# Performance work log

Hardware: AMD Instinct MI355X
Metric: run time of the kernel (lower is better)

Reference implementation:

```python
import jax, jax.numpy as jnp
import numpy as np

N_NODES = 100000
N_EDGES = 1600000
D = 64


def setup_inputs() -> dict:
    key = jax.random.key(0)
    k1, k2, k3 = jax.random.split(key, 3)
    x = jax.random.normal(k1, (N_NODES, D), dtype=jnp.float32)
    edge_index = jax.random.randint(k2, (2, N_EDGES), 0, N_NODES, dtype=jnp.int32)
    W = jax.random.normal(k3, (D, D), dtype=jnp.float32) * 0.05  # linear weight [out_dim, in_dim]
    b = jnp.zeros((D,), dtype=jnp.float32)
    return {"x": x, "edge_index": edge_index, "W": W, "b": b}


def reference(x, edge_index, W, b):
    n = x.shape[0]
    # add self loops
    loops = jnp.arange(n, dtype=edge_index.dtype)
    src = jnp.concatenate([edge_index[0], loops])
    dst = jnp.concatenate([edge_index[1], loops])
    # in-degree (counting self loops) via scatter-add of ones onto dst
    deg = jax.ops.segment_sum(jnp.ones_like(src, dtype=x.dtype), dst, num_segments=n)
    deg_inv_sqrt = jnp.where(deg > 0, jax.lax.rsqrt(jnp.maximum(deg, 1.0)) * (deg > 0), 0.0)
    deg_inv_sqrt = jnp.where(deg > 0, deg ** -0.5, 0.0)
    # per-edge symmetric normalization, gather-scale-scatter
    norm = deg_inv_sqrt[src] * deg_inv_sqrt[dst]  # [E+N]
    msgs = x[src] * norm[:, None]                  # [E+N, D] big irregular gather
    out = jax.ops.segment_sum(msgs, dst, num_segments=n)  # scatter-add to nodes
    # dense linear
    return out @ W.T + b
```

## Files before the change

kernel.cpp:

```cpp
#include <hip/hip_runtime.h>


#define BSHIFT 7
#define BNODES 128
#define CAP 3072
#define EPB 4096
#define SMEM_BYTES 32768

__device__ inline unsigned short f2b_rn(float f) {
    unsigned u = __float_as_uint(f);
    unsigned r = u + 0x7FFFu + ((u >> 16) & 1u);
    return (unsigned short)(r >> 16);
}
__device__ inline float b2f(unsigned short h) {
    return __uint_as_float(((unsigned)h) << 16);
}

__global__ __launch_bounds__(256) void fused_gemm_scatter_kernel(
    const float* __restrict__ x, const float* __restrict__ W,
    ushort4* __restrict__ yh,
    const int* __restrict__ ei, int* __restrict__ gcur,
    unsigned int* __restrict__ grec,
    int n, int e, int nbuck, int sblocks) {
    __shared__ __align__(16) unsigned char smem[SMEM_BYTES];
    int t = threadIdx.x;

    if ((int)blockIdx.x < sblocks) {
        unsigned int* lrec = (unsigned int*)smem;
        unsigned short* lbk = (unsigned short*)(smem + 16384);
        int* lh = (int*)(smem + 24576);
        int* lbase = lh + nbuck;
        for (int i = t; i < nbuck; i += 256) lh[i] = 0;
        __syncthreads();
        int e0 = blockIdx.x * EPB;
        int m = e - e0;
        if (m > EPB) m = EPB;
        for (int i = t; i < m; i += 256) {
            int g = e0 + i;
            int s = ei[g];
            int d = ei[e + g];
            int b = d >> BSHIFT;
            lrec[i] = ((unsigned int)s << BSHIFT) | (unsigned int)(d & (BNODES - 1));
            lbk[i] = (unsigned short)b;
            atomicAdd(&lh[b], 1);
        }
        __syncthreads();
        for (int b = t; b < nbuck; b += 256) {
            int c = lh[b];
            lbase[b] = c ? atomicAdd(&gcur[b], c) : 0;
            lh[b] = 0;
        }
        __syncthreads();
        for (int i = t; i < m; i += 256) {
            int b = lbk[i];
            int pos = lbase[b] + atomicAdd(&lh[b], 1);
            if (pos < CAP)
                grec[(size_t)b * CAP + pos] = lrec[i];
        }
    } else {
        float4* At4 = (float4*)smem;
        float4* Wt4 = (float4*)(smem + 16384);
        int m0 = ((int)blockIdx.x - sblocks) * 64;

#pragma unroll
        for (int j = 0; j < 4; ++j) {
            int idx = t + j * 256;
            int k = idx & 63;
            int r = idx >> 6;
            float4 wv;
            wv.x = W[(size_t)(4 * r + 0) * 64 + k];
            wv.y = W[(size_t)(4 * r + 1) * 64 + k];
            wv.z = W[(size_t)(4 * r + 2) * 64 + k];
            wv.w = W[(size_t)(4 * r + 3) * 64 + k];
            Wt4[k * 16 + (r ^ (k & 15))] = wv;
            float4 av;
            int gm = m0 + 4 * r;
            av.x = (gm + 0 < n) ? x[(size_t)(gm + 0) * 64 + k] : 0.f;
            av.y = (gm + 1 < n) ? x[(size_t)(gm + 1) * 64 + k] : 0.f;
            av.z = (gm + 2 < n) ? x[(size_t)(gm + 2) * 64 + k] : 0.f;
            av.w = (gm + 3 < n) ? x[(size_t)(gm + 3) * 64 + k] : 0.f;
            At4[k * 16 + (r ^ (k & 15))] = av;
        }
        __syncthreads();

        int tx = t & 15, ty = t >> 4;
        float acc[4][4];
#pragma unroll
        for (int i = 0; i < 4; ++i)
#pragma unroll
            for (int j = 0; j < 4; ++j) acc[i][j] = 0.f;

#pragma unroll 8
        for (int k = 0; k < 64; ++k) {
            float4 a = At4[k * 16 + (ty ^ (k & 15))];
            float4 w = Wt4[k * 16 + (tx ^ (k & 15))];
            float av[4] = {a.x, a.y, a.z, a.w};
            float wv[4] = {w.x, w.y, w.z, w.w};
#pragma unroll
            for (int i = 0; i < 4; ++i)
#pragma unroll
                for (int j = 0; j < 4; ++j) acc[i][j] += av[i] * wv[j];
        }

#pragma unroll
        for (int i = 0; i < 4; ++i) {
            int gm = m0 + ty * 4 + i;
            if (gm < n) {
                ushort4 h;
                h.x = f2b_rn(acc[i][0]);
                h.y = f2b_rn(acc[i][1]);
                h.z = f2b_rn(acc[i][2]);
                h.w = f2b_rn(acc[i][3]);
                yh[(size_t)gm * 16 + tx] = h;
            }
        }
    }
}

__global__ __launch_bounds__(256) void dnorm_kernel(
    const unsigned int* __restrict__ grec, const int* __restrict__ gcur,
    float* __restrict__ dnorm, int n) {
    __shared__ int lh[BNODES];
    int t = threadIdx.x;
    int b = blockIdx.x;
    size_t base = (size_t)b * CAP;
    int cnt = gcur[b];
    if (cnt > CAP) cnt = CAP;
    if (t < BNODES) lh[t] = 0;
    __syncthreads();
    for (int i = t; i < cnt; i += 256)
        atomicAdd(&lh[grec[base + i] & (BNODES - 1)], 1);
    __syncthreads();
    if (t < BNODES) {
        int node = (b << BSHIFT) + t;
        if (node < n) dnorm[node] = rsqrtf((float)lh[t] + 1.0f);
    }
}

__global__ __launch_bounds__(512, 4) void csr_gather_kernel(
    const unsigned int* __restrict__ grec, const int* __restrict__ gcur,
    const ushort4* __restrict__ yh, const float* __restrict__ dnorm,
    const float* __restrict__ bias,
    float4* __restrict__ out, int n) {
    __shared__ unsigned int sorted[CAP];
    __shared__ int lh[BNODES];
    __shared__ int ls[BNODES + 1];
    __shared__ int wtot;
    int t = threadIdx.x;
    int b = blockIdx.x;
    size_t base = (size_t)b * CAP;
    int cnt = gcur[b];
    if (cnt > CAP) cnt = CAP;
    int node0 = b << BSHIFT;

    if (t < BNODES) lh[t] = 0;
    __syncthreads();
    for (int i = t; i < cnt; i += 512)
        atomicAdd(&lh[grec[base + i] & (BNODES - 1)], 1);
    __syncthreads();
    int c = 0, ex = 0;
    if (t < BNODES) {
        c = lh[t];
        int lane64 = t & 63;
        int v = c;
#pragma unroll
        for (int o = 1; o < 64; o <<= 1) {
            int u = __shfl_up(v, o, 64);
            if (lane64 >= o) v += u;
        }
        if (t == 63) wtot = v;
        ex = v - c;
    }
    __syncthreads();
    if (t >= 64 && t < BNODES) ex += wtot;
    if (t < BNODES) {
        ls[t] = ex;
        lh[t] = 0;
        if (t == BNODES - 1) ls[BNODES] = ex + c;
    }
    __syncthreads();
    for (int i = t; i < cnt; i += 512) {
        unsigned int r = grec[base + i];
        int nd = r & (BNODES - 1);
        int pos = ls[nd] + atomicAdd(&lh[nd], 1);
        sorted[pos] = r >> BSHIFT;
    }
    __syncthreads();

    int wave = t >> 6;
    int lane = t & 63;
    int grp = lane >> 4;
    int fq = lane & 15;
    float4 bb = ((const float4*)bias)[fq];
    for (int i = 0; i < 16; ++i) {
        int nd = wave * 16 + i;
        int node = node0 + nd;
        if (node >= n) break;
        int beg = ls[nd];
        int end = ls[nd + 1];
        float dn = rsqrtf((float)(end - beg) + 1.0f);
        float4 acc = {0.f, 0.f, 0.f, 0.f};
        if (grp == 0) {
            ushort4 h = yh[(size_t)node * 16 + fq];
            acc.x = dn * b2f(h.x); acc.y = dn * b2f(h.y);
            acc.z = dn * b2f(h.z); acc.w = dn * b2f(h.w);
        }
        int j = beg + grp;
        for (; j + 12 < end; j += 16) {
            int s0 = (int)sorted[j];
            int s1 = (int)sorted[j + 4];
            int s2 = (int)sorted[j + 8];
            int s3 = (int)sorted[j + 12];
            ushort4 h0 = yh[(size_t)s0 * 16 + fq];
            ushort4 h1 = yh[(size_t)s1 * 16 + fq];
            ushort4 h2 = yh[(size_t)s2 * 16 + fq];
            ushort4 h3 = yh[(size_t)s3 * 16 + fq];
            float d0 = dnorm[s0];
            float d1 = dnorm[s1];
            float d2 = dnorm[s2];
            float d3 = dnorm[s3];
            acc.x += d0 * b2f(h0.x); acc.x += d1 * b2f(h1.x);
            acc.x += d2 * b2f(h2.x); acc.x += d3 * b2f(h3.x);
            acc.y += d0 * b2f(h0.y); acc.y += d1 * b2f(h1.y);
            acc.y += d2 * b2f(h2.y); acc.y += d3 * b2f(h3.y);
            acc.z += d0 * b2f(h0.z); acc.z += d1 * b2f(h1.z);
            acc.z += d2 * b2f(h2.z); acc.z += d3 * b2f(h3.z);
            acc.w += d0 * b2f(h0.w); acc.w += d1 * b2f(h1.w);
            acc.w += d2 * b2f(h2.w); acc.w += d3 * b2f(h3.w);
        }
        for (; j < end; j += 4) {
            int s = (int)sorted[j];
            ushort4 h = yh[(size_t)s * 16 + fq];
            float d0 = dnorm[s];
            acc.x += d0 * b2f(h.x); acc.y += d0 * b2f(h.y);
            acc.z += d0 * b2f(h.z); acc.w += d0 * b2f(h.w);
        }
        for (int m = 16; m < 64; m <<= 1) {
            acc.x += __shfl_xor(acc.x, m);
            acc.y += __shfl_xor(acc.y, m);
            acc.z += __shfl_xor(acc.z, m);
            acc.w += __shfl_xor(acc.w, m);
        }
        if (lane < 16) {
            float4 o;
            o.x = acc.x * dn + bb.x;
            o.y = acc.y * dn + bb.y;
            o.z = acc.z * dn + bb.z;
            o.w = acc.w * dn + bb.w;
            out[(size_t)node * 16 + lane] = o;
        }
    }
}

extern "C" void kernel_launch(void* const* d_in, const int* in_sizes, int n_in,
                              void* d_out, int out_size, void* d_ws, size_t ws_size,
                              hipStream_t stream) {
    const float* x    = (const float*)d_in[0];
    const int*   ei   = (const int*)d_in[1];
    const float* W    = (const float*)d_in[2];
    const float* bias = (const float*)d_in[3];
    float* out = (float*)d_out;

    int n = in_sizes[0] / 64;
    int e = in_sizes[1] / 2;
    int nbuck = (n + BNODES - 1) / BNODES;

    auto align = [](size_t v) { return (v + 255) & ~(size_t)255; };
    char* p = (char*)d_ws;
    int* gcur = (int*)p;                    p += align((size_t)nbuck * 4);
    unsigned int* grec = (unsigned int*)p;  p += align((size_t)nbuck * CAP * 4);
    float* dnorm = (float*)p;               p += align((size_t)n * 4);
    ushort4* yh = (ushort4*)p;

    int sblocks = (e + EPB - 1) / EPB;
    int gblocks = (n + 63) / 64;

    hipMemsetAsync(gcur, 0, (size_t)nbuck * 4, stream);
    fused_gemm_scatter_kernel<<<sblocks + gblocks, 256, 0, stream>>>(
        x, W, yh, ei, gcur, grec, n, e, nbuck, sblocks);
    dnorm_kernel<<<nbuck, 256, 0, stream>>>(grec, gcur, dnorm, n);
    csr_gather_kernel<<<nbuck, 512, 0, stream>>>(grec, gcur, yh, dnorm, bias,
                                                 (float4*)out, n);
}
```

Baseline: 165.9 us.

## Compute dense x·Wᵀ with split-bf16 MFMA instead of shared-memory FP32 FMA

Replaces the LDS-tiled FP32 FMA GEMM in the transform blocks with 16x16x32 bf16 MFMA instructions. Each operand is split into a hi/lo bf16 pair and three MFMAs are issued so the result stays close to FP32 accuracy. Operands now load straight from global memory into registers, removing the shared-memory staging and the block barrier. This trades scalar FMA work for matrix-core throughput, at the cost of extra split arithmetic and W being reloaded per wave.

```diff
diff --git a/kernel.cpp b/kernel.cpp
--- a/kernel.cpp
+++ b/kernel.cpp
@@ -7,6 +7,9 @@
 #define EPB 4096
 #define SMEM_BYTES 32768
 
+typedef short bf16x8 __attribute__((ext_vector_type(8)));
+typedef float f32x4 __attribute__((ext_vector_type(4)));
+
 __device__ inline unsigned short f2b_rn(float f) {
     unsigned u = __float_as_uint(f);
     unsigned r = u + 0x7FFFu + ((u >> 16) & 1u);
@@ -14,6 +17,24 @@
 }
 __device__ inline float b2f(unsigned short h) {
     return __uint_as_float(((unsigned)h) << 16);
+}
+
+__device__ inline void split8(float4 a, float4 b, bf16x8* hi, bf16x8* lo) {
+    float f[8] = {a.x, a.y, a.z, a.w, b.x, b.y, b.z, b.w};
+    union U { unsigned u[4]; bf16x8 v; } uh, ul;
+#pragma unroll
+    for (int i = 0; i < 4; ++i) {
+        unsigned u0 = __float_as_uint(f[2 * i]);
+        unsigned u1 = __float_as_uint(f[2 * i + 1]);
+        uh.u[i] = (u0 >> 16) | (u1 & 0xFFFF0000u);
+        float r0 = f[2 * i]     - __uint_as_float(u0 & 0xFFFF0000u);
+        float r1 = f[2 * i + 1] - __uint_as_float(u1 & 0xFFFF0000u);
+        unsigned v0 = __float_as_uint(r0);
+        unsigned v1 = __float_as_uint(r1);
+        ul.u[i] = (v0 >> 16) | (v1 & 0xFFFF0000u);
+    }
+    *hi = uh.v;
+    *lo = ul.v;
 }
 
 __global__ __launch_bounds__(256) void fused_gemm_scatter_kernel(
@@ -58,60 +79,46 @@
                 grec[(size_t)b * CAP + pos] = lrec[i];
         }
     } else {
-        float4* At4 = (float4*)smem;
-        float4* Wt4 = (float4*)(smem + 16384);
-        int m0 = ((int)blockIdx.x - sblocks) * 64;
-
-#pragma unroll
-        for (int j = 0; j < 4; ++j) {
-            int idx = t + j * 256;
-            int k = idx & 63;
-            int r = idx >> 6;
-            float4 wv;
-            wv.x = W[(size_t)(4 * r + 0) * 64 + k];
-            wv.y = W[(size_t)(4 * r + 1) * 64 + k];
-            wv.z = W[(size_t)(4 * r + 2) * 64 + k];
-            wv.w = W[(size_t)(4 * r + 3) * 64 + k];
-            Wt4[k * 16 + (r ^ (k & 15))] = wv;
-            float4 av;
-            int gm = m0 + 4 * r;
-            av.x = (gm + 0 < n) ? x[(size_t)(gm + 0) * 64 + k] : 0.f;
-            av.y = (gm + 1 < n) ? x[(size_t)(gm + 1) * 64 + k] : 0.f;
-            av.z = (gm + 2 < n) ? x[(size_t)(gm + 2) * 64 + k] : 0.f;
-            av.w = (gm + 3 < n) ? x[(size_t)(gm + 3) * 64 + k] : 0.f;
-            At4[k * 16 + (r ^ (k & 15))] = av;
-        }
-        __syncthreads();
-
-        int tx = t & 15, ty = t >> 4;
-        float acc[4][4];
-#pragma unroll
-        for (int i = 0; i < 4; ++i)
-#pragma unroll
-            for (int j = 0; j < 4; ++j) acc[i][j] = 0.f;
-
-#pragma unroll 8
-        for (int k = 0; k < 64; ++k) {
-            float4 a = At4[k * 16 + (ty ^ (k & 15))];
-            float4 w = Wt4[k * 16 + (tx ^ (k & 15))];
-            float av[4] = {a.x, a.y, a.z, a.w};
-            float wv[4] = {w.x, w.y, w.z, w.w};
-#pragma unroll
-            for (int i = 0; i < 4; ++i)
-#pragma unroll
-                for (int j = 0; j < 4; ++j) acc[i][j] += av[i] * wv[j];
-        }
-
-#pragma unroll
-        for (int i = 0; i < 4; ++i) {
-            int gm = m0 + ty * 4 + i;
-            if (gm < n) {
+        int wave = t >> 6, lane = t & 63;
+        int jn = lane & 15;
+        int g = lane >> 4;
+        int node = ((int)blockIdx.x - sblocks) * 64 + wave * 16 + jn;
+
+        bf16x8 xhi[2], xlo[2];
+#pragma unroll
+        for (int kb = 0; kb < 2; ++kb) {
+            float4 p0 = {0.f, 0.f, 0.f, 0.f}, p1 = {0.f, 0.f, 0.f, 0.f};
+            if (node < n) {
+                const float4* xp =
+                    (const float4*)(x + (size_t)node * 64 + kb * 32 + g * 8);
+                p0 = xp[0];
+                p1 = xp[1];
+            }
+            split8(p0, p1, &xhi[kb], &xlo[kb]);
+        }
+
+#pragma unroll
+        for (int tt = 0; tt < 4; ++tt) {
+            f32x4 acc = {0.f, 0.f, 0.f, 0.f};
+#pragma unroll
+            for (int kb = 0; kb < 2; ++kb) {
+                const float4* wp =
+                    (const float4*)(W + (size_t)(tt * 16 + jn) * 64 + kb * 32 + g * 8);
+                float4 q0 = wp[0];
+                float4 q1 = wp[1];
+                bf16x8 whi, wlo;
+                split8(q0, q1, &whi, &wlo);
+                acc = __builtin_amdgcn_mfma_f32_16x16x32_bf16(wlo, xhi[kb], acc, 0, 0, 0);
+                acc = __builtin_amdgcn_mfma_f32_16x16x32_bf16(whi, xlo[kb], acc, 0, 0, 0);
+                acc = __builtin_amdgcn_mfma_f32_16x16x32_bf16(whi, xhi[kb], acc, 0, 0, 0);
+            }
+            if (node < n) {
                 ushort4 h;
-                h.x = f2b_rn(acc[i][0]);
-                h.y = f2b_rn(acc[i][1]);
-                h.z = f2b_rn(acc[i][2]);
-                h.w = f2b_rn(acc[i][3]);
-                yh[(size_t)gm * 16 + tx] = h;
+                h.x = f2b_rn(acc[0]);
+                h.y = f2b_rn(acc[1]);
+                h.z = f2b_rn(acc[2]);
+                h.w = f2b_rn(acc[3]);
+                yh[(size_t)node * 16 + (tt * 4 + g)] = h;
             }
         }
     }
```

After: 163.2 us. Within noise of the previous version (-1.6%).
